# Kernel tuning notes

Hardware: AMD Instinct MI355X
Metric: run time of the kernel (lower is better)

## Reference

```python
import jax, jax.numpy as jnp
import numpy as np
from jax import lax

LEVEL = 128  # level_num

def _bn(x, g, b, m, v):
    # inference-mode BatchNorm, channel axis = 1
    sh = (1, -1) + (1,) * (x.ndim - 2)
    return (x - m.reshape(sh)) * (g.reshape(sh) * lax.rsqrt(v.reshape(sh) + 1e-5)) + b.reshape(sh)

def _leaky(a):
    return jnp.where(a > 0, a, 0.01 * a)

def _l2n(a):
    return a / jnp.maximum(jnp.linalg.norm(a, axis=1, keepdims=True), 1e-12)

def _resize_bilinear_ac(x, oh, ow):
    # bilinear, align_corners=True, NCHW
    n, c, h, w = x.shape
    ys = jnp.linspace(0.0, h - 1.0, oh)
    xs = jnp.linspace(0.0, w - 1.0, ow)
    y0 = jnp.floor(ys).astype(jnp.int32)
    x0 = jnp.floor(xs).astype(jnp.int32)
    y1 = jnp.minimum(y0 + 1, h - 1)
    x1 = jnp.minimum(x0 + 1, w - 1)
    wy = (ys - y0)[:, None]
    wx = (xs - x0)[None, :]
    Y0, Y1, X0, X1 = y0[:, None], y1[:, None], x0[None, :], x1[None, :]
    return (x[:, :, Y0, X0] * (1 - wy) * (1 - wx) + x[:, :, Y0, X1] * (1 - wy) * wx
            + x[:, :, Y1, X0] * wy * (1 - wx) + x[:, :, Y1, X1] * wy * wx)

def _forward(x, conv1_w, bn1_g, bn1_b, bn1_m, bn1_v, conv2_w, f1_w, f2_w, f2_g, f2_b, f2_m, f2_v,
             out1_w, out1_g, out1_b, out1_m, out1_v, k_w, q_w, v_w, out_w, out_g, out_b, out_m, out_v):
    # conv1: 3x3 conv + BN + LeakyReLU
    y = lax.conv_general_dilated(x, conv1_w, (1, 1), 'SAME', dimension_numbers=('NCHW', 'OIHW', 'NCHW'))
    y = _leaky(_bn(y, bn1_g, bn1_b, bn1_m, bn1_v))
    # conv2: 1x1 conv, 256->128
    x2 = jnp.einsum('nchw,oc->nohw', y, conv2_w)
    N, C, H, W = x2.shape  # C = 128
    x_ave = x2.mean(axis=(2, 3), keepdims=True)  # [N,C,1,1]
    cos = (_l2n(x_ave) * _l2n(x2)).sum(1)        # [N,H,W]
    sh, sw = H // 3, W // 3
    L = sh * sw
    # H,W divisible by 3 -> adaptive_avg_pool2d is identity
    cs = cos.reshape(N, 3, sh, 3, sw).transpose(0, 1, 3, 2, 4).reshape(N, 9, L).transpose(0, 2, 1)  # [N,L,9]
    # LBP bit packing vs center (index 4); weight 0 at index 4 (strict > gives 0 there)
    bits = (cs > cs[:, :, 4:5]).astype(x.dtype)
    wts = jnp.array([1, 2, 4, 8, 0, 16, 32, 64, 128], dtype=x.dtype)
    code = (bits * wts).sum(-1)  # [N,L]
    mn = code.min(-1, keepdims=True)
    mx = code.max(-1, keepdims=True)
    code = (code - mn) / (mx - mn)
    cmin = code.min(-1, keepdims=True)
    cmax = code.max(-1, keepdims=True)
    qlv = (2 * jnp.arange(LEVEL, dtype=x.dtype) + 1) / (2 * LEVEL) * (cmax - cmin) + cmin  # [N,LEVEL]
    inter = (qlv[:, 1] - qlv[:, 0])[:, None, None]  # [N,1,1]
    quant = 1 - jnp.abs(qlv[:, None, :] - code[:, :, None])  # [N,L,LEVEL]
    quant = jnp.where(quant > 1 - inter, quant, 0.0)
    sta = quant.sum(1)                                       # [N,LEVEL]
    sta = sta / sta.sum(-1, keepdims=True)
    sta2 = jnp.stack([qlv, sta], axis=1)                     # [N,2,LEVEL]
    h1 = _leaky(jnp.einsum('ncl,oc->nol', sta2, f1_w))       # f1: 2->64
    h2 = jax.nn.relu(_bn(jnp.einsum('ncl,oc->nol', h1, f2_w), f2_g, f2_b, f2_m, f2_v))  # f2: 64->128
    xa = jnp.broadcast_to(x_ave[:, :, 0, 0][:, :, None], (N, C, LEVEL))
    s = jnp.concatenate([h2, xa], axis=1)                    # [N,256,LEVEL]
    s = jax.nn.relu(_bn(jnp.einsum('ncl,oc->nol', s, out1_w), out1_g, out1_b, out1_m, out1_v))
    k = jnp.einsum('ncl,oc->nol', s, k_w)
    q = jnp.einsum('ncl,oc->nol', s, q_w)
    v = jnp.einsum('ncl,oc->nol', s, v_w)
    w = jax.nn.softmax(jnp.einsum('ncl,ncm->nlm', k, q), axis=-1)  # bmm(k^T, q)
    f = jnp.einsum('nlm,ncm->ncl', w, v)                            # bmm(w, v^T) then transpose
    f = jax.nn.relu(_bn(jnp.einsum('ncl,oc->nol', f, out_w), out_g, out_b, out_m, out_v))
    out = jnp.einsum('ncl,npl->ncp', f, quant).reshape(N, 256, sh, sh)  # bmm(f, quant^T)
    return _resize_bilinear_ac(out, H, W)

def setup_inputs() -> dict:
    key = jax.random.key(0)
    ks = jax.random.split(key, 16)
    f32 = jnp.float32
    def nrm(k, shape, s=0.05):
        return s * jax.random.normal(k, shape, f32)
    def bnp(k, c):
        k1, k2, k3, k4 = jax.random.split(k, 4)
        return (1.0 + 0.1 * jax.random.normal(k1, (c,), f32),
                0.1 * jax.random.normal(k2, (c,), f32),
                0.1 * jax.random.normal(k3, (c,), f32),
                jax.random.uniform(k4, (c,), f32, 0.5, 1.5))
    d = {}
    d['x'] = jax.random.normal(ks[0], (32, 512, 48, 48), f32)
    d['conv1_w'] = nrm(ks[1], (256, 512, 3, 3))
    d['bn1_g'], d['bn1_b'], d['bn1_m'], d['bn1_v'] = bnp(ks[2], 256)
    d['conv2_w'] = nrm(ks[3], (128, 256))
    d['f1_w'] = nrm(ks[4], (64, 2), 0.3)
    d['f2_w'] = nrm(ks[5], (128, 64), 0.1)
    d['f2_g'], d['f2_b'], d['f2_m'], d['f2_v'] = bnp(ks[6], 128)
    d['out1_w'] = nrm(ks[7], (256, 256))
    d['out1_g'], d['out1_b'], d['out1_m'], d['out1_v'] = bnp(ks[8], 256)
    d['k_w'] = nrm(ks[9], (256, 256))
    d['q_w'] = nrm(ks[10], (256, 256))
    d['v_w'] = nrm(ks[11], (256, 256))
    d['out_w'] = nrm(ks[12], (256, 256))
    d['out_g'], d['out_b'], d['out_m'], d['out_v'] = bnp(ks[13], 256)
    return d

def reference(x, conv1_w, bn1_g, bn1_b, bn1_m, bn1_v, conv2_w, f1_w, f2_w, f2_g, f2_b, f2_m, f2_v,
              out1_w, out1_g, out1_b, out1_m, out1_v, k_w, q_w, v_w, out_w, out_g, out_b, out_m, out_v):
    return _forward(x, conv1_w, bn1_g, bn1_b, bn1_m, bn1_v, conv2_w, f1_w, f2_w, f2_g, f2_b, f2_m, f2_v,
                    out1_w, out1_g, out1_b, out1_m, out1_v, k_w, q_w, v_w, out_w, out_g, out_b, out_m, out_v)
```

## Files before the change

### kernel.cpp

```cpp
#include <hip/hip_runtime.h>
#include <math.h>

#define N_IMG 32
#define P2304 2304
#define CIN 512
#define CMID 256
#define C2 128
#define LEV 128

typedef _Float16 half8 __attribute__((ext_vector_type(8)));
typedef float f32x16 __attribute__((ext_vector_type(16)));

__device__ __forceinline__ float wredSum(float v){
#pragma unroll
  for (int o = 32; o > 0; o >>= 1) v += __shfl_down(v, o, 64);
  return v;
}
__device__ __forceinline__ float wredMax(float v){
#pragma unroll
  for (int o = 32; o > 0; o >>= 1) v = fmaxf(v, __shfl_down(v, o, 64));
  return v;
}
__device__ __forceinline__ float wredMin(float v){
#pragma unroll
  for (int o = 32; o > 0; o >>= 1) v = fminf(v, __shfl_down(v, o, 64));
  return v;
}

__global__ void prep_w1_kernel(const float* __restrict__ w1,
                               uint4* __restrict__ Wh, uint4* __restrict__ Wl){
  int fid = blockIdx.x * 256 + threadIdx.x;
  int lam = fid & 63;
  int c32 = (fid >> 6) & 3;
  int cot = (fid >> 8) & 1;
  int kt  = fid >> 9;
  int co = cot * 128 + c32 * 32 + (lam & 31);
  half8 vh, vl;
#pragma unroll
  for (int j = 0; j < 8; ++j){
    int k = kt * 16 + ((lam >> 5) << 3) + j;
    int r = k >> 9;
    int ci = k & 511;
    float v = w1[co * (CIN * 9) + ci * 9 + r];
    _Float16 h = (_Float16)v;
    vh[j] = h;
    vl[j] = (_Float16)((v - (float)h) * 2048.0f);
  }
  Wh[fid] = *(uint4*)&vh;
  Wl[fid] = *(uint4*)&vl;
}

__global__ void prep_w2_kernel(const float* __restrict__ w2,
                               uint4* __restrict__ Wh, uint4* __restrict__ Wl){
  int fid = blockIdx.x * 256 + threadIdx.x;
  int lam = fid & 63;
  int c32 = (fid >> 6) & 3;
  int kt  = fid >> 8;
  int co = c32 * 32 + (lam & 31);
  half8 vh, vl;
#pragma unroll
  for (int j = 0; j < 8; ++j){
    int k = kt * 16 + ((lam >> 5) << 3) + j;
    float v = w2[co * CMID + k];
    _Float16 h = (_Float16)v;
    vh[j] = h;
    vl[j] = (_Float16)((v - (float)h) * 2048.0f);
  }
  Wh[fid] = *(uint4*)&vh;
  Wl[fid] = *(uint4*)&vl;
}

__global__ void prep_bn_kernel(const float* __restrict__ g1, const float* __restrict__ b1,
                               const float* __restrict__ m1, const float* __restrict__ v1,
                               float* __restrict__ s1, float* __restrict__ t1){
  int c = threadIdx.x;
  float s = g1[c] * (1.0f / sqrtf(v1[c] + 1e-5f));
  s1[c] = s;
  t1[c] = b1[c] - m1[c] * s;
}

template<int R, int CPT, int COTN, bool BN>
__global__ __launch_bounds__(256, 2) void conv_mfma_kernel(
    const float* __restrict__ in, const uint4* __restrict__ Wh, const uint4* __restrict__ Wl,
    const float* __restrict__ s1, const float* __restrict__ t1, float* __restrict__ out)
{
  __shared__ _Float16 Abuf[2][2][2][2048];
  __shared__ _Float16 Bbuf[2][2][2][2048];
  const int t = threadIdx.x;
  const int lam = t & 63;
  const int g = t >> 6;

  int n, pt_blk, cot;
  if (COTN == 2){
    int xcd = blockIdx.x & 7;
    int rest = blockIdx.x >> 3;
    n = xcd * 4 + rest / 36;
    int inner = rest % 36;
    pt_blk = inner % 18;
    cot = inner / 18;
  } else {
    pt_blk = blockIdx.x % 18;
    cot = 0;
    n = blockIdx.x / 18;
  }
  const int pbase = pt_blk * 128;
  const int cobase = cot * 128;

  const int khi = lam >> 5;
  const int pp = (g << 5) + (lam & 31);
  const int p = pbase + pp;
  const int ph = p / 48, pw = p - ph * 48;
  const float* in_n = in + (size_t)n * CPT * P2304;

  const int S = (R * CPT) / 32;
  const int KTPT = CPT / 16;

  f32x16 acc_hh[2][2], acc_x[2][2];
#pragma unroll
  for (int a = 0; a < 2; ++a)
#pragma unroll
    for (int b = 0; b < 2; ++b){
#pragma unroll
      for (int e = 0; e < 16; ++e){ acc_hh[a][b][e] = 0.f; acc_x[a][b][e] = 0.f; }
    }

  uint4 rAh[2], rAl[2];
  float rB[16];
  bool vmask;

#define ISSUE(SV)                                                             \
  {                                                                           \
    int s_ = (SV);                                                            \
    _Pragma("unroll")                                                         \
    for (int kf = 0; kf < 2; ++kf){                                           \
      int fi = (((2 * s_ + kf) * COTN + cot) * 4 + g) * 64 + lam;             \
      rAh[kf] = Wh[fi];                                                       \
      rAl[kf] = Wl[fi];                                                       \
    }                                                                         \
    int r_ = (R == 1) ? 0 : ((2 * s_) / KTPT);                                \
    int cbase_ = ((2 * s_) % KTPT) * 16;                                      \
    int dh_ = (R == 1) ? 0 : (r_ / 3 - 1);                                    \
    int dw_ = (R == 1) ? 0 : (r_ - (r_ / 3) * 3 - 1);                         \
    int hh_ = ph + dh_, ww_ = pw + dw_;                                       \
    vmask = ((unsigned)hh_ < 48u) & ((unsigned)ww_ < 48u);                    \
    int hc_ = min(max(hh_, 0), 47), wc_ = min(max(ww_, 0), 47);               \
    const float* src_ = in_n + hc_ * 48 + wc_                                 \
                        + (size_t)(cbase_ + khi * 8) * P2304;                 \
    _Pragma("unroll")                                                         \
    for (int kf = 0; kf < 2; ++kf)                                            \
      _Pragma("unroll")                                                       \
      for (int j = 0; j < 8; ++j)                                             \
        rB[kf * 8 + j] = src_[(kf * 16 + j) * P2304];                         \
  }

#define STASH(NXT)                                                            \
  {                                                                           \
    _Pragma("unroll")                                                         \
    for (int kf = 0; kf < 2; ++kf){                                           \
      *(uint4*)&Abuf[NXT][kf][0][t * 8] = rAh[kf];                            \
      *(uint4*)&Abuf[NXT][kf][1][t * 8] = rAl[kf];                            \
      half8 vh, vl;                                                           \
      _Pragma("unroll")                                                       \
      for (int j = 0; j < 8; ++j){                                            \
        float v = vmask ? rB[kf * 8 + j] : 0.0f;                              \
        _Float16 h = (_Float16)v;                                             \
        vh[j] = h;                                                            \
        vl[j] = (_Float16)((v - (float)h) * 2048.0f);                         \
      }                                                                       \
      *(half8*)&Bbuf[NXT][kf][0][t * 8] = vh;                                 \
      *(half8*)&Bbuf[NXT][kf][1][t * 8] = vl;                                 \
    }                                                                         \
  }

#define COMPUTE(CUR, KF)                                                      \
  {                                                                           \
    const int ct0 = (g & 1) * 2, pt0 = (g >> 1) * 2;                          \
    half8 fAh[2], fAl[2], fBh[2], fBl[2];                                     \
    _Pragma("unroll")                                                         \
    for (int a = 0; a < 2; ++a){                                              \
      fAh[a] = *(half8*)&Abuf[CUR][KF][0][(ct0 + a) * 512 + lam * 8];         \
      fAl[a] = *(half8*)&Abuf[CUR][KF][1][(ct0 + a) * 512 + lam * 8];         \
      fBh[a] = *(half8*)&Bbuf[CUR][KF][0][(pt0 + a) * 512 + lam * 8];         \
      fBl[a] = *(half8*)&Bbuf[CUR][KF][1][(pt0 + a) * 512 + lam * 8];         \
    }                                                                         \
    _Pragma("unroll")                                                         \
    for (int a = 0; a < 2; ++a)                                               \
      _Pragma("unroll")                                                       \
      for (int b = 0; b < 2; ++b){                                            \
        acc_hh[a][b] = __builtin_amdgcn_mfma_f32_32x32x16_f16(                \
            fAh[a], fBh[b], acc_hh[a][b], 0, 0, 0);                           \
        acc_x[a][b] = __builtin_amdgcn_mfma_f32_32x32x16_f16(                 \
            fAh[a], fBl[b], acc_x[a][b], 0, 0, 0);                            \
        acc_x[a][b] = __builtin_amdgcn_mfma_f32_32x32x16_f16(                 \
            fAl[a], fBh[b], acc_x[a][b], 0, 0, 0);                            \
      }                                                                       \
  }

  ISSUE(0);
  STASH(0);
  __syncthreads();

  for (int s = 0; s < S; ++s){
    const int cur = s & 1, nxt = cur ^ 1;
    const bool more = (s + 1 < S);
    if (more) ISSUE(s + 1);
    COMPUTE(cur, 0);
    if (more) STASH(nxt);
    COMPUTE(cur, 1);
    __syncthreads();
  }
#undef ISSUE
#undef STASH
#undef COMPUTE

  const int M = COTN * 128;
#pragma unroll
  for (int a = 0; a < 2; ++a){
    const int ctile = (g & 1) * 2 + a;
#pragma unroll
    for (int b = 0; b < 2; ++b){
      const int ptile = (g >> 1) * 2 + b;
      const int pg = pbase + ptile * 32 + (lam & 31);
#pragma unroll
      for (int rg = 0; rg < 16; ++rg){
        const int row = (rg & 3) + 8 * (rg >> 2) + 4 * (lam >> 5);
        const int co = cobase + ctile * 32 + row;
        float val = acc_hh[a][b][rg] + acc_x[a][b][rg] * (1.0f / 2048.0f);
        if (BN){
          val = val * s1[co] + t1[co];
          val = val > 0.f ? val : 0.01f * val;
        }
        out[((size_t)n * M + co) * P2304 + pg] = val;
      }
    }
  }
}

__global__ void xave_kernel(const float* __restrict__ x2, float* __restrict__ xave){
  __shared__ float red[4];
  int nc = blockIdx.x, t = threadIdx.x;
  const float* row = x2 + nc * P2304;
  float s = 0.f;
#pragma unroll
  for (int i = 0; i < 9; i++) s += row[t + 256 * i];
  float w = wredSum(s);
  if ((t & 63) == 0) red[t >> 6] = w;
  __syncthreads();
  if (t == 0) xave[nc] = (red[0] + red[1] + red[2] + red[3]) * (1.0f / 2304.0f);
}

__global__ void xan_kernel(const float* __restrict__ xave, float* __restrict__ xan){
  __shared__ float red[2];
  int n = blockIdx.x, t = threadIdx.x;
  float v = xave[n * 128 + t];
  float w = wredSum(v * v);
  if ((t & 63) == 0) red[t >> 6] = w;
  __syncthreads();
  float norm = fmaxf(sqrtf(red[0] + red[1]), 1e-12f);
  xan[n * 128 + t] = v / norm;
}

__global__ void cos_kernel(const float* __restrict__ x2, const float* __restrict__ xan,
                           float* __restrict__ cosb){
  int idx = blockIdx.x * 256 + threadIdx.x;
  if (idx >= N_IMG * P2304) return;
  int n = idx / P2304;
  int p = idx - n * P2304;
  const float* xp = x2 + n * C2 * P2304 + p;
  const float* an = xan + n * 128;
  float dot = 0.f, ss = 0.f;
  for (int c = 0; c < 128; c++){
    float v = xp[c * P2304];
    dot += an[c] * v;
    ss  += v * v;
  }
  cosb[idx] = dot / fmaxf(sqrtf(ss), 1e-12f);
}

__global__ void lbp_kernel(const float* __restrict__ cosb, float* __restrict__ code,
                           float* __restrict__ qlv){
  __shared__ float red[4];
  int n = blockIdx.x;
  int l = threadIdx.x;
  int ir = l >> 4, ic = l & 15;
  const float* cn = cosb + n * P2304;
  float cs4 = cn[(16 + ir) * 48 + (16 + ic)];
  const float wts[9] = {1.f, 2.f, 4.f, 8.f, 0.f, 16.f, 32.f, 64.f, 128.f};
  float codev = 0.f;
#pragma unroll
  for (int j = 0; j < 9; j++){
    int jr = j / 3, jc = j - 3 * (j / 3);
    float vv = cn[(jr * 16 + ir) * 48 + (jc * 16 + ic)];
    if (vv > cs4) codev += wts[j];
  }
  float w;
  w = wredMin(codev);
  if ((l & 63) == 0) red[l >> 6] = w;
  __syncthreads();
  float mn = fminf(fminf(red[0], red[1]), fminf(red[2], red[3]));
  __syncthreads();
  w = wredMax(codev);
  if ((l & 63) == 0) red[l >> 6] = w;
  __syncthreads();
  float mx = fmaxf(fmaxf(red[0], red[1]), fmaxf(red[2], red[3]));
  __syncthreads();
  float cd = (codev - mn) / (mx - mn);
  w = wredMin(cd);
  if ((l & 63) == 0) red[l >> 6] = w;
  __syncthreads();
  float cmin = fminf(fminf(red[0], red[1]), fminf(red[2], red[3]));
  __syncthreads();
  w = wredMax(cd);
  if ((l & 63) == 0) red[l >> 6] = w;
  __syncthreads();
  float cmax = fmaxf(fmaxf(red[0], red[1]), fmaxf(red[2], red[3]));
  code[n * 256 + l] = cd;
  if (l < 128){
    float tmp = (float)(2 * l + 1) * (1.0f / 256.0f);
    qlv[n * 128 + l] = tmp * (cmax - cmin) + cmin;
  }
}

__global__ void quant_kernel(const float* __restrict__ code, const float* __restrict__ qlv,
                             float* __restrict__ quantT){
  __shared__ float cs[256];
  __shared__ float qs[128];
  int n = blockIdx.x, t = threadIdx.x;
  cs[t] = code[n * 256 + t];
  if (t < 128) qs[t] = qlv[n * 128 + t];
  __syncthreads();
  float thr = 1.0f - (qs[1] - qs[0]);
  float* dst = quantT + n * LEV * 256;
#pragma unroll 4
  for (int i = 0; i < 128; i++){
    int v = t + 256 * i;
    int lv = v >> 8;
    int p = v & 255;
    float qq = 1.0f - fabsf(qs[lv] - cs[p]);
    dst[v] = (qq > thr) ? qq : 0.f;
  }
}

__global__ void sta_kernel(const float* __restrict__ quantT, float* __restrict__ sta){
  __shared__ float red[2];
  int n = blockIdx.x, i = threadIdx.x;
  const float* qr = quantT + (n * LEV + i) * 256;
  float s = 0.f;
  for (int p = 0; p < 256; p++) s += qr[p];
  float w = wredSum(s);
  if ((i & 63) == 0) red[i >> 6] = w;
  __syncthreads();
  float tot = red[0] + red[1];
  sta[n * 128 + i] = s / tot;
}

__global__ void h1_kernel(const float* __restrict__ f1w, const float* __restrict__ qlv,
                          const float* __restrict__ sta, float* __restrict__ h1){
  int idx = blockIdx.x * 256 + threadIdx.x;
  if (idx >= N_IMG * 64 * 128) return;
  int l = idx & 127;
  int n = idx >> 13;
  int o = (idx >> 7) & 63;
  float a = f1w[o * 2] * qlv[n * 128 + l] + f1w[o * 2 + 1] * sta[n * 128 + l];
  h1[idx] = a > 0.f ? a : 0.01f * a;
}

__global__ void gemm_w_kernel(const float* __restrict__ Wm, const float* __restrict__ B,
                              float* __restrict__ Cout, int Cdim, int O, int total, int mode,
                              const float* __restrict__ g, const float* __restrict__ bb,
                              const float* __restrict__ mm, const float* __restrict__ vv){
  int idx = blockIdx.x * 256 + threadIdx.x;
  if (idx >= total) return;
  int per_n = (O >> 2) << 7;
  int n = idx / per_n;
  int rem = idx - n * per_n;
  int o0 = (rem >> 7) << 2;
  int l = rem & 127;
  const float* Bn = B + (n * Cdim) * 128 + l;
  const float* w0 = Wm + (o0 + 0) * Cdim;
  const float* w1 = Wm + (o0 + 1) * Cdim;
  const float* w2 = Wm + (o0 + 2) * Cdim;
  const float* w3 = Wm + (o0 + 3) * Cdim;
  float a0 = 0, a1 = 0, a2 = 0, a3 = 0;
  for (int c = 0; c < Cdim; c++){
    float bv = Bn[c * 128];
    a0 += w0[c] * bv; a1 += w1[c] * bv; a2 += w2[c] * bv; a3 += w3[c] * bv;
  }
  float av[4] = {a0, a1, a2, a3};
#pragma unroll
  for (int j = 0; j < 4; j++){
    int o = o0 + j;
    float val = av[j];
    if (mode == 1){
      float s = g[o] * (1.0f / sqrtf(vv[o] + 1e-5f));
      val = (val - mm[o]) * s + bb[o];
      val = fmaxf(val, 0.f);
    }
    Cout[(n * O + o) * 128 + l] = val;
  }
}

__global__ void concat_kernel(const float* __restrict__ h2, const float* __restrict__ xave,
                              float* __restrict__ s){
  int idx = blockIdx.x * 256 + threadIdx.x;
  if (idx >= N_IMG * 256 * 128) return;
  int l = idx & 127;
  int c = (idx >> 7) & 255;
  int n = idx >> 15;
  s[idx] = (c < 128) ? h2[(n * 128 + c) * 128 + l] : xave[n * 128 + (c - 128)];
}

__global__ void attn_sc_kernel(const float* __restrict__ k, const float* __restrict__ q,
                               float* __restrict__ sc){
  int idx = blockIdx.x * 256 + threadIdx.x;
  if (idx >= N_IMG * 32 * 128) return;
  int m = idx & 127;
  int l0 = ((idx >> 7) & 31) << 2;
  int n = idx >> 12;
  const float* kn = k + n * 256 * 128;
  const float* qn = q + n * 256 * 128 + m;
  float a0 = 0, a1 = 0, a2 = 0, a3 = 0;
  for (int c = 0; c < 256; c++){
    float qv = qn[c * 128];
    const float* kr = kn + c * 128 + l0;
    a0 += kr[0] * qv; a1 += kr[1] * qv; a2 += kr[2] * qv; a3 += kr[3] * qv;
  }
  float* dst = sc + (n * 128 + l0) * 128 + m;
  dst[0] = a0; dst[128] = a1; dst[256] = a2; dst[384] = a3;
}

__global__ void softmax_kernel(float* __restrict__ sc){
  __shared__ float red[2];
  int row = blockIdx.x;
  int t = threadIdx.x;
  float v = sc[row * 128 + t];
  float w = wredMax(v);
  if ((t & 63) == 0) red[t >> 6] = w;
  __syncthreads();
  float mx = fmaxf(red[0], red[1]);
  float e = expf(v - mx);
  float s = wredSum(e);
  __syncthreads();
  if ((t & 63) == 0) red[t >> 6] = s;
  __syncthreads();
  sc[row * 128 + t] = e / (red[0] + red[1]);
}

__global__ void transpose_sc_kernel(const float* __restrict__ sc, float* __restrict__ scT){
  int idx = blockIdx.x * 256 + threadIdx.x;
  if (idx >= N_IMG * 128 * 128) return;
  int l = idx & 127;
  int m = (idx >> 7) & 127;
  int n = idx >> 14;
  scT[idx] = sc[(n * 128 + l) * 128 + m];
}

__global__ void attn_f_kernel(const float* __restrict__ vb, const float* __restrict__ scT,
                              float* __restrict__ f){
  int idx = blockIdx.x * 256 + threadIdx.x;
  if (idx >= N_IMG * 64 * 128) return;
  int l = idx & 127;
  int c0 = ((idx >> 7) & 63) << 2;
  int n = idx >> 13;
  const float* vn = vb + (n * 256 + c0) * 128;
  const float* sn = scT + n * 128 * 128 + l;
  float a0 = 0, a1 = 0, a2 = 0, a3 = 0;
  for (int m = 0; m < 128; m++){
    float sv = sn[m * 128];
    a0 += vn[m] * sv; a1 += vn[128 + m] * sv; a2 += vn[256 + m] * sv; a3 += vn[384 + m] * sv;
  }
  float* dst = f + (n * 256 + c0) * 128 + l;
  dst[0] = a0; dst[128] = a1; dst[256] = a2; dst[384] = a3;
}

__global__ void final_kernel(const float* __restrict__ g, const float* __restrict__ quantT,
                             float* __restrict__ outs){
  int idx = blockIdx.x * 256 + threadIdx.x;
  if (idx >= N_IMG * 64 * 256) return;
  int p = idx & 255;
  int c0 = ((idx >> 8) & 63) << 2;
  int n = idx >> 14;
  const float* gn = g + (n * 256 + c0) * 128;
  const float* qn = quantT + (n * LEV) * 256 + p;
  float a0 = 0, a1 = 0, a2 = 0, a3 = 0;
  for (int lv = 0; lv < 128; lv++){
    float qv = qn[lv * 256];
    a0 += gn[lv] * qv; a1 += gn[128 + lv] * qv; a2 += gn[256 + lv] * qv; a3 += gn[384 + lv] * qv;
  }
  float* dst = outs + (n * 256 + c0) * 256 + p;
  dst[0] = a0; dst[256] = a1; dst[512] = a2; dst[768] = a3;
}

__global__ void resize_kernel(const float* __restrict__ outs, float* __restrict__ dout){
  int idx = blockIdx.x * 256 + threadIdx.x;
  if (idx >= N_IMG * 256 * P2304) return;
  int ow = idx % 48;
  int tmp = idx / 48;
  int oh = tmp % 48;
  int nc = tmp / 48;
  const float* src = outs + nc * 256;
  float fy = oh * (15.0f / 47.0f);
  float fx = ow * (15.0f / 47.0f);
  int y0 = (int)fy;
  int x0 = (int)fx;
  int y1 = min(y0 + 1, 15);
  int x1 = min(x0 + 1, 15);
  float wy = fy - (float)y0;
  float wx = fx - (float)x0;
  float v00 = src[y0 * 16 + x0], v01 = src[y0 * 16 + x1];
  float v10 = src[y1 * 16 + x0], v11 = src[y1 * 16 + x1];
  dout[idx] = v00 * (1.f - wy) * (1.f - wx) + v01 * (1.f - wy) * wx
            + v10 * wy * (1.f - wx) + v11 * wy * wx;
}

extern "C" void kernel_launch(void* const* d_in, const int* in_sizes, int n_in,
                              void* d_out, int out_size, void* d_ws, size_t ws_size,
                              hipStream_t stream)
{
  const float* x       = (const float*)d_in[0];
  const float* conv1_w = (const float*)d_in[1];
  const float* bn1_g   = (const float*)d_in[2];
  const float* bn1_b   = (const float*)d_in[3];
  const float* bn1_m   = (const float*)d_in[4];
  const float* bn1_v   = (const float*)d_in[5];
  const float* conv2_w = (const float*)d_in[6];
  const float* f1_w    = (const float*)d_in[7];
  const float* f2_w    = (const float*)d_in[8];
  const float* f2_g    = (const float*)d_in[9];
  const float* f2_b    = (const float*)d_in[10];
  const float* f2_m    = (const float*)d_in[11];
  const float* f2_v    = (const float*)d_in[12];
  const float* out1_w  = (const float*)d_in[13];
  const float* out1_g  = (const float*)d_in[14];
  const float* out1_b  = (const float*)d_in[15];
  const float* out1_m  = (const float*)d_in[16];
  const float* out1_v  = (const float*)d_in[17];
  const float* k_w     = (const float*)d_in[18];
  const float* q_w     = (const float*)d_in[19];
  const float* v_w     = (const float*)d_in[20];
  const float* out_w   = (const float*)d_in[21];
  const float* out_g   = (const float*)d_in[22];
  const float* out_b   = (const float*)d_in[23];
  const float* out_m   = (const float*)d_in[24];
  const float* out_v   = (const float*)d_in[25];

  float* ws = (float*)d_ws;
  float* dout = (float*)d_out;

  float* w_y   = ws;
  float* w_x2  = ws + 18874368;
  float* w_W1h = ws + 28311552;
  float* w_W1l = ws + 28901376;
  float* w_W2h = ws + 29491200;
  float* w_W2l = ws + 29507584;
  float* w_s1  = ws + 29523968;
  float* w_t1  = ws + 29524224;
  float* w_xave = w_y + 0;
  float* w_xan  = w_y + 4096;
  float* w_cos  = w_y + 8192;
  float* w_code = w_y + 81920;
  float* w_qlv  = w_y + 90112;
  float* w_sta  = w_y + 94208;
  float* w_quant= w_y + 98304;
  float* w_h1   = w_y + 1146880;
  float* w_h2   = w_y + 1409024;
  float* w_s    = w_y + 1933312;
  float* w_k    = w_y + 2981888;
  float* w_q    = w_y + 4030464;
  float* w_v    = w_y + 5079040;
  float* w_sc   = w_y + 6127616;
  float* w_scT  = w_y + 6651904;
  float* w_f    = w_y + 7176192;
  float* w_g    = w_y + 8224768;
  float* w_outs = w_y + 9273344;
  float* w_s2   = w_y + 11370496;

  prep_w1_kernel<<<576, 256, 0, stream>>>(conv1_w, (uint4*)w_W1h, (uint4*)w_W1l);
  prep_w2_kernel<<<16, 256, 0, stream>>>(conv2_w, (uint4*)w_W2h, (uint4*)w_W2l);
  prep_bn_kernel<<<1, 256, 0, stream>>>(bn1_g, bn1_b, bn1_m, bn1_v, w_s1, w_t1);

  conv_mfma_kernel<9, 512, 2, true><<<1152, 256, 0, stream>>>(
      x, (const uint4*)w_W1h, (const uint4*)w_W1l, w_s1, w_t1, w_y);
  conv_mfma_kernel<1, 256, 1, false><<<576, 256, 0, stream>>>(
      w_y, (const uint4*)w_W2h, (const uint4*)w_W2l, w_s1, w_t1, w_x2);

  xave_kernel<<<4096, 256, 0, stream>>>(w_x2, w_xave);
  xan_kernel<<<32, 128, 0, stream>>>(w_xave, w_xan);
  cos_kernel<<<288, 256, 0, stream>>>(w_x2, w_xan, w_cos);
  lbp_kernel<<<32, 256, 0, stream>>>(w_cos, w_code, w_qlv);
  quant_kernel<<<32, 256, 0, stream>>>(w_code, w_qlv, w_quant);
  sta_kernel<<<32, 128, 0, stream>>>(w_quant, w_sta);
  h1_kernel<<<1024, 256, 0, stream>>>(f1_w, w_qlv, w_sta, w_h1);
  gemm_w_kernel<<<512, 256, 0, stream>>>(f2_w, w_h1, w_h2, 64, 128, N_IMG * 32 * 128, 1,
                                         f2_g, f2_b, f2_m, f2_v);
  concat_kernel<<<4096, 256, 0, stream>>>(w_h2, w_xave, w_s);
  gemm_w_kernel<<<1024, 256, 0, stream>>>(out1_w, w_s, w_s2, 256, 256, N_IMG * 64 * 128, 1,
                                          out1_g, out1_b, out1_m, out1_v);
  gemm_w_kernel<<<1024, 256, 0, stream>>>(k_w, w_s2, w_k, 256, 256, N_IMG * 64 * 128, 0,
                                          nullptr, nullptr, nullptr, nullptr);
  gemm_w_kernel<<<1024, 256, 0, stream>>>(q_w, w_s2, w_q, 256, 256, N_IMG * 64 * 128, 0,
                                          nullptr, nullptr, nullptr, nullptr);
  gemm_w_kernel<<<1024, 256, 0, stream>>>(v_w, w_s2, w_v, 256, 256, N_IMG * 64 * 128, 0,
                                          nullptr, nullptr, nullptr, nullptr);
  attn_sc_kernel<<<512, 256, 0, stream>>>(w_k, w_q, w_sc);
  softmax_kernel<<<4096, 128, 0, stream>>>(w_sc);
  transpose_sc_kernel<<<2048, 256, 0, stream>>>(w_sc, w_scT);
  attn_f_kernel<<<1024, 256, 0, stream>>>(w_v, w_scT, w_f);
  gemm_w_kernel<<<1024, 256, 0, stream>>>(out_w, w_f, w_g, 256, 256, N_IMG * 64 * 128, 1,
                                          out_g, out_b, out_m, out_v);
  final_kernel<<<2048, 256, 0, stream>>>(w_g, w_quant, w_outs);
  resize_kernel<<<73728, 256, 0, stream>>>(w_outs, dout);
}
```

Measured before the change: 1.511 ms.

## Pre-split conv1 input into padded fp16 hi/lo and stream tiles via LDS DMA

Adds a presplit kernel that converts the input into zero-padded fp16 hi/lo pairs, laid out channel-group major. A new conv1 kernel then loads both weights and activations straight into shared memory with global_load_lds. This removes per-thread register staging, the fp32-to-fp16 split and the boundary masking from the conv1 inner loop. Images are processed in chunks sized to the available workspace, which costs an extra global write and read of the split input and may add launches when the workspace is small.

```diff
diff --git a/kernel.cpp b/kernel.cpp
--- a/kernel.cpp
+++ b/kernel.cpp
@@ -10,6 +10,12 @@
 
 typedef _Float16 half8 __attribute__((ext_vector_type(8)));
 typedef float f32x16 __attribute__((ext_vector_type(16)));
+
+__device__ __forceinline__ void async16(const void* gsrc, void* ldsdst){
+  __builtin_amdgcn_global_load_lds(
+      (const __attribute__((address_space(1))) void*)gsrc,
+      (__attribute__((address_space(3))) void*)ldsdst, 16, 0, 0);
+}
 
 __device__ __forceinline__ float wredSum(float v){
 #pragma unroll
@@ -77,6 +83,135 @@
   float s = g1[c] * (1.0f / sqrtf(v1[c] + 1e-5f));
   s1[c] = s;
   t1[c] = b1[c] - m1[c] * s;
+}
+
+__global__ void presplit_kernel(const float* __restrict__ x, int n0, int nimg,
+                                uint4* __restrict__ xh, uint4* __restrict__ xl){
+  int idx = blockIdx.x * 256 + threadIdx.x;
+  if (idx >= nimg * 64 * 2500) return;
+  int pp = idx % 2500;
+  int cc = (idx / 2500) & 63;
+  int nl = idx / (2500 * 64);
+  int hrow = pp / 50;
+  int h = hrow - 1, w = pp - hrow * 50 - 1;
+  half8 vh = {0, 0, 0, 0, 0, 0, 0, 0};
+  half8 vl = {0, 0, 0, 0, 0, 0, 0, 0};
+  if ((unsigned)h < 48u && (unsigned)w < 48u){
+    const float* src = x + ((size_t)(n0 + nl) * CIN + cc * 8) * P2304 + h * 48 + w;
+#pragma unroll
+    for (int j = 0; j < 8; ++j){
+      float v = src[(size_t)j * P2304];
+      _Float16 hh = (_Float16)v;
+      vh[j] = hh;
+      vl[j] = (_Float16)((v - (float)hh) * 2048.0f);
+    }
+  }
+  xh[idx] = *(uint4*)&vh;
+  xl[idx] = *(uint4*)&vl;
+}
+
+__global__ __launch_bounds__(256, 2) void conv1_dma_kernel(
+    const uint4* __restrict__ xh, const uint4* __restrict__ xl,
+    const uint4* __restrict__ Wh, const uint4* __restrict__ Wl,
+    const float* __restrict__ s1, const float* __restrict__ t1,
+    float* __restrict__ out, int n0)
+{
+  __shared__ _Float16 Abuf[2][2][2][2048];
+  __shared__ _Float16 Bbuf[2][2][2][2048];
+  const int t = threadIdx.x, lam = t & 63, g = t >> 6;
+  const int bid = blockIdx.x;
+  const int n_l = bid / 36, inner = bid % 36;
+  const int pt_blk = inner % 18, cot = inner / 18;
+  const int pbase = pt_blk * 128, cobase = cot * 128;
+  const int khi = lam >> 5;
+  const int pp = (g << 5) + (lam & 31);
+  const int p = pbase + pp;
+  const int ph = p / 48, pw = p - ph * 48;
+  const int padbase = (ph + 1) * 50 + pw + 1;
+  const int nbase = n_l * 64 * 2500;
+
+  f32x16 acc_hh[2][2], acc_x[2][2];
+#pragma unroll
+  for (int a = 0; a < 2; ++a)
+#pragma unroll
+    for (int b = 0; b < 2; ++b){
+#pragma unroll
+      for (int e = 0; e < 16; ++e){ acc_hh[a][b][e] = 0.f; acc_x[a][b][e] = 0.f; }
+    }
+
+#define STG(SV, BF)                                                           \
+  {                                                                           \
+    int s_ = (SV);                                                            \
+    int r_ = s_ >> 4;                                                         \
+    int r3_ = r_ / 3;                                                         \
+    int dlt = (r3_ - 1) * 50 + (r_ - r3_ * 3 - 1);                            \
+    _Pragma("unroll")                                                         \
+    for (int kf = 0; kf < 2; ++kf){                                           \
+      int kt = 2 * s_ + kf;                                                   \
+      int fi = ((kt * 2 + cot) * 4 + g) * 64 + lam;                           \
+      async16(Wh + fi, &Abuf[BF][kf][0][g * 512]);                            \
+      async16(Wl + fi, &Abuf[BF][kf][1][g * 512]);                            \
+      int cc = ((s_ & 15) << 2) + (kf << 1) + khi;                            \
+      int bi = nbase + cc * 2500 + padbase + dlt;                             \
+      async16(xh + bi, &Bbuf[BF][kf][0][g * 512]);                            \
+      async16(xl + bi, &Bbuf[BF][kf][1][g * 512]);                            \
+    }                                                                         \
+  }
+
+#define CMP(CUR, KF)                                                          \
+  {                                                                           \
+    const int ct0 = (g & 1) * 2, pt0 = (g >> 1) * 2;                          \
+    half8 fAh[2], fAl[2], fBh[2], fBl[2];                                     \
+    _Pragma("unroll")                                                         \
+    for (int a = 0; a < 2; ++a){                                              \
+      fAh[a] = *(half8*)&Abuf[CUR][KF][0][(ct0 + a) * 512 + lam * 8];         \
+      fAl[a] = *(half8*)&Abuf[CUR][KF][1][(ct0 + a) * 512 + lam * 8];         \
+      fBh[a] = *(half8*)&Bbuf[CUR][KF][0][(pt0 + a) * 512 + lam * 8];         \
+      fBl[a] = *(half8*)&Bbuf[CUR][KF][1][(pt0 + a) * 512 + lam * 8];         \
+    }                                                                         \
+    _Pragma("unroll")                                                         \
+    for (int a = 0; a < 2; ++a)                                               \
+      _Pragma("unroll")                                                       \
+      for (int b = 0; b < 2; ++b){                                            \
+        acc_hh[a][b] = __builtin_amdgcn_mfma_f32_32x32x16_f16(                \
+            fAh[a], fBh[b], acc_hh[a][b], 0, 0, 0);                           \
+        acc_x[a][b] = __builtin_amdgcn_mfma_f32_32x32x16_f16(                 \
+            fAh[a], fBl[b], acc_x[a][b], 0, 0, 0);                            \
+        acc_x[a][b] = __builtin_amdgcn_mfma_f32_32x32x16_f16(                 \
+            fAl[a], fBh[b], acc_x[a][b], 0, 0, 0);                            \
+      }                                                                       \
+  }
+
+  STG(0, 0);
+  __syncthreads();
+  for (int s = 0; s < 144; ++s){
+    const int cur = s & 1;
+    if (s + 1 < 144) STG(s + 1, cur ^ 1);
+    CMP(cur, 0);
+    CMP(cur, 1);
+    __syncthreads();
+  }
+#undef STG
+#undef CMP
+
+#pragma unroll
+  for (int a = 0; a < 2; ++a){
+    const int ctile = (g & 1) * 2 + a;
+#pragma unroll
+    for (int b = 0; b < 2; ++b){
+      const int ptile = (g >> 1) * 2 + b;
+      const int pg = pbase + ptile * 32 + (lam & 31);
+#pragma unroll
+      for (int rg = 0; rg < 16; ++rg){
+        const int row = (rg & 3) + 8 * (rg >> 2) + 4 * (lam >> 5);
+        const int co = cobase + ctile * 32 + row;
+        float val = acc_hh[a][b][rg] + acc_x[a][b][rg] * (1.0f / 2048.0f);
+        val = val * s1[co] + t1[co];
+        val = val > 0.f ? val : 0.01f * val;
+        out[((size_t)(n0 + n_l) * CMID + co) * P2304 + pg] = val;
+      }
+    }
+  }
 }
 
 template<int R, int CPT, int COTN, bool BN>
@@ -165,7 +300,7 @@
         float v = vmask ? rB[kf * 8 + j] : 0.0f;                              \
         _Float16 h = (_Float16)v;                                             \
         vh[j] = h;                                                            \
-        vl[j] = (_Float16)((v - (float)h) * 2048.0f);                         \
+        vl[j] = (_Float16)((v - (float)h) * 2048.0f);                        \
       }                                                                       \
       *(half8*)&Bbuf[NXT][kf][0][t * 8] = vh;                                 \
       *(half8*)&Bbuf[NXT][kf][1][t * 8] = vl;                                 \
@@ -547,14 +682,30 @@
   float* ws = (float*)d_ws;
   float* dout = (float*)d_out;
 
+  size_t favail = ws_size >> 2;
+  int nimg = 4;
+  if (favail >= 61047296) nimg = 32;
+  else if (favail >= 40567296) nimg = 16;
+  else if (favail >= 30327296) nimg = 8;
+  const int NC = 32 / nimg;
+
+  const size_t F_Y = 18874368;
+  size_t xkF = (size_t)nimg * 1280000;
+  size_t reg2 = xkF > 9437184 ? xkF : (size_t)9437184;
+
   float* w_y   = ws;
-  float* w_x2  = ws + 18874368;
-  float* w_W1h = ws + 28311552;
-  float* w_W1l = ws + 28901376;
-  float* w_W2h = ws + 29491200;
-  float* w_W2l = ws + 29507584;
-  float* w_s1  = ws + 29523968;
-  float* w_t1  = ws + 29524224;
+  float* w_xk  = ws + F_Y;
+  float* w_x2  = w_xk;
+  uint4* xkh   = (uint4*)w_xk;
+  uint4* xkl   = xkh + (size_t)nimg * 160000;
+  float* w_wbk = ws + F_Y + reg2;
+  float* w_W1h = w_wbk;
+  float* w_W1l = w_wbk + 589824;
+  float* w_W2h = w_wbk + 1179648;
+  float* w_W2l = w_wbk + 1196032;
+  float* w_s1  = w_wbk + 1212416;
+  float* w_t1  = w_wbk + 1212672;
+
   float* w_xave = w_y + 0;
   float* w_xan  = w_y + 4096;
   float* w_cos  = w_y + 8192;
@@ -579,8 +730,11 @@
   prep_w2_kernel<<<16, 256, 0, stream>>>(conv2_w, (uint4*)w_W2h, (uint4*)w_W2l);
   prep_bn_kernel<<<1, 256, 0, stream>>>(bn1_g, bn1_b, bn1_m, bn1_v, w_s1, w_t1);
 
-  conv_mfma_kernel<9, 512, 2, true><<<1152, 256, 0, stream>>>(
-      x, (const uint4*)w_W1h, (const uint4*)w_W1l, w_s1, w_t1, w_y);
+  for (int c = 0; c < NC; ++c){
+    presplit_kernel<<<nimg * 625, 256, 0, stream>>>(x, c * nimg, nimg, xkh, xkl);
+    conv1_dma_kernel<<<nimg * 36, 256, 0, stream>>>(
+        xkh, xkl, (const uint4*)w_W1h, (const uint4*)w_W1l, w_s1, w_t1, w_y, c * nimg);
+  }
   conv_mfma_kernel<1, 256, 1, false><<<576, 256, 0, stream>>>(
       w_y, (const uint4*)w_W2h, (const uint4*)w_W2l, w_s1, w_t1, w_x2);
 
```

Measured after the change: 1.569 ms. 3.8% more time.
